# Optimization experiments

Measured on AMD Instinct MI355X. Metric: run time of the kernel, lower is better.

The kernel has to match this reference:

```python
import jax, jax.numpy as jnp
import numpy as np
import math

NUM_WORDS = 8192
WORD_WIDTH = 512
PROJ_WIDTH = 64
NUM_HEADS = 8
SCALE_FACTOR = 100.0

def setup_inputs() -> dict:
    key = jax.random.key(0)
    kx, kq, kk, kv, ko = jax.random.split(key, 5)
    x = jax.random.normal(kx, (NUM_WORDS, WORD_WIDTH), dtype=jnp.float32)
    w_q = jax.random.normal(kq, (WORD_WIDTH, PROJ_WIDTH), dtype=jnp.float32) / SCALE_FACTOR
    w_k = jax.random.normal(kk, (WORD_WIDTH, PROJ_WIDTH), dtype=jnp.float32) / SCALE_FACTOR
    w_v = jax.random.normal(kv, (WORD_WIDTH, PROJ_WIDTH), dtype=jnp.float32) / SCALE_FACTOR
    w_o = jax.random.normal(ko, (WORD_WIDTH, WORD_WIDTH), dtype=jnp.float32)
    return {"x": x, "w_q": w_q, "w_k": w_k, "w_v": w_v, "w_o": w_o}

def reference(x, w_q, w_k, w_v, w_o):
    # Single self-attention head (all 8 heads in the source share the same weights).
    q = x @ w_q            # [N, P]
    k = x @ w_k            # [N, P]
    v = x @ w_v            # [N, P]
    scores = jax.nn.softmax((q @ k.T) / jnp.sqrt(jnp.float32(q.shape[1])), axis=1)  # [N, N]
    head = scores @ v      # [N, P]
    # concat of NUM_HEADS identical head outputs along dim=1
    concat = jnp.tile(head, (1, NUM_HEADS))  # [N, NUM_HEADS*P]
    return concat @ w_o    # [N, WORD_WIDTH]
```

## Files before the change

kernel.cpp:

```cpp
#include <hip/hip_runtime.h>
#include <stdint.h>

#define N_WORDS 8192
#define LOG2E_8 0.18033688011112043f

typedef __attribute__((ext_vector_type(8))) short short8;
typedef __attribute__((ext_vector_type(4))) float f32x4;
typedef __attribute__((ext_vector_type(2))) __fp16 pkhalf2;
typedef __attribute__((ext_vector_type(4))) _Float16 half4;
typedef __attribute__((ext_vector_type(8))) _Float16 half8;

__device__ __forceinline__ unsigned short f32_to_bf16(float f) {
    union { float f; unsigned u; } v; v.f = f;
    unsigned u = v.u;
    return (unsigned short)((u + 0x7FFFu + ((u >> 16) & 1u)) >> 16);
}

__device__ __forceinline__ unsigned short f32_to_f16(float f) {
    union { _Float16 h; unsigned short u; } cv;
    cv.h = (_Float16)f;
    return cv.u;
}

__device__ __forceinline__ void async16(const void* g, void* l) {
    __builtin_amdgcn_global_load_lds(
        (const __attribute__((address_space(1))) unsigned int*)g,
        (__attribute__((address_space(3))) unsigned int*)l, 16, 0, 0);
}

__global__ __launch_bounds__(256) void qkv_gemm(
    const float* __restrict__ x,
    const float* __restrict__ wq, const float* __restrict__ wk,
    const float* __restrict__ wv, const float* __restrict__ wo,
    unsigned short* __restrict__ qB, unsigned short* __restrict__ kB,
    unsigned short* __restrict__ vH, float* __restrict__ we)
{
    int t = threadIdx.x;
    int mat = blockIdx.y;

    if (mat == 3) {
        int i = blockIdx.x * 256 + t;
        int p = i >> 9;
        int j = i & 511;
        float s = 0.0f;
#pragma unroll
        for (int h = 0; h < 8; ++h) s += wo[(size_t)(h * 64 + p) * 512 + j];
        we[i] = s;
        return;
    }

    __shared__ __align__(16) unsigned short ldsX[64 * 72];
    __shared__ __align__(16) unsigned short ldsW[64 * 72];

    int mt = blockIdx.x;
    const float* w = (mat == 0) ? wq : (mat == 1) ? wk : wv;

    int wvid = t >> 6, lane = t & 63;
    int lq = lane & 15, quad = lane >> 4;

    f32x4 acc[4];
#pragma unroll
    for (int nt = 0; nt < 4; ++nt) acc[nt] = (f32x4){0.f, 0.f, 0.f, 0.f};

    float4 xr[4];
    float wr[16];
    int wn = t & 63, wkbs = (t >> 6) * 16;

    {
        int k0 = 0;
#pragma unroll
        for (int j2 = 0; j2 < 4; ++j2) {
            int i = t + j2 * 256;
            int row = i >> 4, c4 = (i & 15) * 4;
            xr[j2] = *(const float4*)(x + (size_t)(mt * 64 + row) * 512 + k0 + c4);
        }
#pragma unroll
        for (int kk = 0; kk < 16; ++kk)
            wr[kk] = w[(size_t)(k0 + wkbs + kk) * 64 + wn];
    }

    for (int kb = 0; kb < 8; ++kb) {
        __syncthreads();
#pragma unroll
        for (int j2 = 0; j2 < 4; ++j2) {
            int i = t + j2 * 256;
            int row = i >> 4, c4 = (i & 15) * 4;
            unsigned p0 = f32_to_bf16(xr[j2].x) | ((unsigned)f32_to_bf16(xr[j2].y) << 16);
            unsigned p1 = f32_to_bf16(xr[j2].z) | ((unsigned)f32_to_bf16(xr[j2].w) << 16);
            *(uint2*)(&ldsX[row * 72 + c4]) = make_uint2(p0, p1);
        }
#pragma unroll
        for (int kk = 0; kk < 16; kk += 2) {
            unsigned p = f32_to_bf16(wr[kk]) | ((unsigned)f32_to_bf16(wr[kk + 1]) << 16);
            *(unsigned*)(&ldsW[wn * 72 + wkbs + kk]) = p;
        }
        __syncthreads();

        if (kb < 7) {
            int k0 = (kb + 1) * 64;
#pragma unroll
            for (int j2 = 0; j2 < 4; ++j2) {
                int i = t + j2 * 256;
                int row = i >> 4, c4 = (i & 15) * 4;
                xr[j2] = *(const float4*)(x + (size_t)(mt * 64 + row) * 512 + k0 + c4);
            }
#pragma unroll
            for (int kk = 0; kk < 16; ++kk)
                wr[kk] = w[(size_t)(k0 + wkbs + kk) * 64 + wn];
        }

        int m = wvid * 16 + lq;
        short8 a0 = *(const short8*)(&ldsX[m * 72 + quad * 8]);
        short8 a1 = *(const short8*)(&ldsX[m * 72 + 32 + quad * 8]);
#pragma unroll
        for (int nt = 0; nt < 4; ++nt) {
            short8 b0 = *(const short8*)(&ldsW[(nt * 16 + lq) * 72 + quad * 8]);
            short8 b1 = *(const short8*)(&ldsW[(nt * 16 + lq) * 72 + 32 + quad * 8]);
            acc[nt] = __builtin_amdgcn_mfma_f32_16x16x32_bf16(a0, b0, acc[nt], 0, 0, 0);
            acc[nt] = __builtin_amdgcn_mfma_f32_16x16x32_bf16(a1, b1, acc[nt], 0, 0, 0);
        }
    }

    int mrow_base = mt * 64 + wvid * 16;
#pragma unroll
    for (int nt = 0; nt < 4; ++nt) {
#pragma unroll
        for (int r = 0; r < 4; ++r) {
            int row = mrow_base + quad * 4 + r;
            int n = nt * 16 + lq;
            float v = acc[nt][r];
            if (mat == 0) {
                v *= LOG2E_8;
                int col = ((((n >> 3) ^ (row & 7)) << 3)) | (n & 7);
                qB[(size_t)row * 64 + col] = f32_to_bf16(v);
            } else if (mat == 1) {
                int col = ((((n >> 3) ^ (row & 7)) << 3)) | (n & 7);
                kB[(size_t)row * 64 + col] = f32_to_bf16(v);
            } else {
                int rs = (row & ~63) | (((((row >> 3) & 7) ^ (n & 7)) << 3)) | (row & 7);
                vH[(size_t)n * N_WORDS + rs] = f32_to_f16(v);
            }
        }
    }
}

__global__ __launch_bounds__(256) void attn_kernel(
    const unsigned short* __restrict__ qB,
    const unsigned short* __restrict__ kB,
    const unsigned short* __restrict__ vH,
    float* __restrict__ pO, float* __restrict__ pl, int nk)
{
    __shared__ __align__(16) unsigned short ldsK[2][128 * 64];
    __shared__ __align__(16) unsigned short ldsV[2][64 * 128];

    int t = threadIdx.x;
    int wvid = t >> 6, lane = t & 63;
    int lq = lane & 15, quad = lane >> 4;
    int mbase = blockIdx.x * 128 + wvid * 32;
    int n0 = blockIdx.y * nk;

    short8 qf[2][2];
#pragma unroll
    for (int qs = 0; qs < 2; ++qs) {
        int row = mbase + qs * 16 + lq;
        const unsigned short* qr = qB + (size_t)row * 64;
        int s7 = row & 7;
        qf[qs][0] = *(const short8*)(qr + ((quad ^ s7) << 3));
        qf[qs][1] = *(const short8*)(qr + (((4 + quad) ^ s7) << 3));
    }

    f32x4 oacc[2][4];
#pragma unroll
    for (int qs = 0; qs < 2; ++qs)
#pragma unroll
        for (int vt = 0; vt < 4; ++vt) oacc[qs][vt] = (f32x4){0.f, 0.f, 0.f, 0.f};
    f32x4 lacc[2];
    lacc[0] = (f32x4){0.f, 0.f, 0.f, 0.f};
    lacc[1] = (f32x4){0.f, 0.f, 0.f, 0.f};

    const half8 ones = {(_Float16)1.f, (_Float16)1.f, (_Float16)1.f, (_Float16)1.f,
                        (_Float16)1.f, (_Float16)1.f, (_Float16)1.f, (_Float16)1.f};

    auto stage = [&](int buf, int nb) {
        const char* gK = (const char*)kB + (size_t)nb * 128;
#pragma unroll
        for (int i = 0; i < 4; ++i) {
            int L0 = (wvid * 4 + i) * 64;
            async16(gK + (size_t)(L0 + lane) * 16, (char*)ldsK[buf] + (size_t)L0 * 16);
        }
#pragma unroll
        for (int i = 0; i < 4; ++i) {
            int L0 = (wvid * 4 + i) * 64;
            int L = L0 + lane;
            int vcol = L >> 4, ct = L & 15;
            const char* src = (const char*)vH + (size_t)vcol * 16384 +
                              (size_t)nb * 2 + ((ct >> 3) << 7) + ((ct & 7) << 4);
            async16(src, (char*)ldsV[buf] + (size_t)L0 * 16);
        }
    };

    int tiles = nk >> 7;
    stage(0, n0);
    int cur = 0;

    for (int tt = 0; tt < tiles; ++tt) {
        __syncthreads();
        if (tt + 1 < tiles) stage(cur ^ 1, n0 + (tt + 1) * 128);

        __builtin_amdgcn_s_setprio(1);
        const unsigned short* K = ldsK[cur];
        const unsigned short* V = ldsV[cur];

#pragma unroll
        for (int u = 0; u < 4; ++u) {
            f32x4 st[2][2];
#pragma unroll
            for (int h = 0; h < 2; ++h) {
                int nt = 2 * u + h;
                int s7 = lq & 7;
                const unsigned short* kr = K + (nt * 16 + lq) * 64;
                short8 a0 = *(const short8*)(kr + ((quad ^ s7) << 3));
                short8 a1 = *(const short8*)(kr + (((4 + quad) ^ s7) << 3));
                f32x4 s0 = (f32x4){0.f, 0.f, 0.f, 0.f};
                f32x4 s1 = (f32x4){0.f, 0.f, 0.f, 0.f};
                s0 = __builtin_amdgcn_mfma_f32_16x16x32_bf16(a0, qf[0][0], s0, 0, 0, 0);
                s0 = __builtin_amdgcn_mfma_f32_16x16x32_bf16(a1, qf[0][1], s0, 0, 0, 0);
                s1 = __builtin_amdgcn_mfma_f32_16x16x32_bf16(a0, qf[1][0], s1, 0, 0, 0);
                s1 = __builtin_amdgcn_mfma_f32_16x16x32_bf16(a1, qf[1][1], s1, 0, 0, 0);
                st[h][0] = s0;
                st[h][1] = s1;
            }

            union { half8 v8; pkhalf2 v2[4]; } pa[2];
#pragma unroll
            for (int qs = 0; qs < 2; ++qs) {
#pragma unroll
                for (int h = 0; h < 2; ++h) {
                    float e0 = exp2f(st[h][qs][0]);
                    float e1 = exp2f(st[h][qs][1]);
                    float e2 = exp2f(st[h][qs][2]);
                    float e3 = exp2f(st[h][qs][3]);
                    pa[qs].v2[h * 2 + 0] = __builtin_amdgcn_cvt_pkrtz(e0, e1);
                    pa[qs].v2[h * 2 + 1] = __builtin_amdgcn_cvt_pkrtz(e2, e3);
                }
                lacc[qs] = __builtin_amdgcn_mfma_f32_16x16x32_f16(
                    pa[qs].v8, ones, lacc[qs], 0, 0, 0);
            }

            int ct0 = 4 * u + (quad >> 1);
            int off = (quad & 1) * 4;
#pragma unroll
            for (int vt = 0; vt < 4; ++vt) {
                int vcol = vt * 16 + lq;
                int cs0 = (ct0 & 8) | ((ct0 & 7) ^ (vcol & 7));
                int ct1 = ct0 + 2;
                int cs1 = (ct1 & 8) | ((ct1 & 7) ^ (vcol & 7));
                union { half8 v8; half4 v4[2]; } vb;
                vb.v4[0] = *(const half4*)(V + vcol * 128 + (cs0 << 3) + off);
                vb.v4[1] = *(const half4*)(V + vcol * 128 + (cs1 << 3) + off);
                oacc[0][vt] = __builtin_amdgcn_mfma_f32_16x16x32_f16(
                    pa[0].v8, vb.v8, oacc[0][vt], 0, 0, 0);
                oacc[1][vt] = __builtin_amdgcn_mfma_f32_16x16x32_f16(
                    pa[1].v8, vb.v8, oacc[1][vt], 0, 0, 0);
            }
        }
        __builtin_amdgcn_s_setprio(0);
        cur ^= 1;
    }

    size_t obase = (size_t)blockIdx.y * N_WORDS;
    if (lq == 0) {
#pragma unroll
        for (int qs = 0; qs < 2; ++qs)
#pragma unroll
            for (int r = 0; r < 4; ++r)
                pl[obase + mbase + qs * 16 + quad * 4 + r] = lacc[qs][r];
    }
#pragma unroll
    for (int qs = 0; qs < 2; ++qs)
#pragma unroll
        for (int vt = 0; vt < 4; ++vt)
#pragma unroll
            for (int r = 0; r < 4; ++r) {
                int row = mbase + qs * 16 + quad * 4 + r;
                pO[(obase + row) * 64 + vt * 16 + lq] = oacc[qs][vt][r];
            }
}

__global__ __launch_bounds__(256) void out_kernel(
    const float* __restrict__ pO, const float* __restrict__ pl,
    const float* __restrict__ we, float* __restrict__ out, int S)
{
    __shared__ __align__(16) float ldsHT[64 * 16];
    int t = threadIdx.x;
    int r0 = blockIdx.x * 16;

#pragma unroll
    for (int j = 0; j < 4; ++j) {
        int i = t + j * 256;
        int row = i >> 6, d = i & 63;
        float so = 0.f, sl = 0.f;
        for (int s = 0; s < S; ++s) {
            so += pO[((size_t)s * N_WORDS + r0 + row) * 64 + d];
            sl += pl[(size_t)s * N_WORDS + r0 + row];
        }
        ldsHT[d * 16 + row] = so / sl;
    }
    __syncthreads();

    int w = t >> 6, l = t & 63;
    int cg = w & 1, rg = w >> 1;
    int j0 = cg * 256 + l * 4;

    float4 acc[8];
#pragma unroll
    for (int rr = 0; rr < 8; ++rr) acc[rr] = (float4){0.f, 0.f, 0.f, 0.f};

    for (int k = 0; k < 64; ++k) {
        float4 wv = *(const float4*)(we + (size_t)k * 512 + j0);
        float4 h0 = *(const float4*)(ldsHT + k * 16 + rg * 8);
        float4 h1 = *(const float4*)(ldsHT + k * 16 + rg * 8 + 4);
        float hr[8] = {h0.x, h0.y, h0.z, h0.w, h1.x, h1.y, h1.z, h1.w};
#pragma unroll
        for (int rr = 0; rr < 8; ++rr) {
            acc[rr].x = fmaf(hr[rr], wv.x, acc[rr].x);
            acc[rr].y = fmaf(hr[rr], wv.y, acc[rr].y);
            acc[rr].z = fmaf(hr[rr], wv.z, acc[rr].z);
            acc[rr].w = fmaf(hr[rr], wv.w, acc[rr].w);
        }
    }

#pragma unroll
    for (int rr = 0; rr < 8; ++rr) {
        int row = r0 + rg * 8 + rr;
        *(float4*)(out + (size_t)row * 512 + j0) = acc[rr];
    }
}

extern "C" void kernel_launch(void* const* d_in, const int* in_sizes, int n_in,
                              void* d_out, int out_size, void* d_ws, size_t ws_size,
                              hipStream_t stream)
{
    const float* x  = (const float*)d_in[0];
    const float* wq = (const float*)d_in[1];
    const float* wk = (const float*)d_in[2];
    const float* wv = (const float*)d_in[3];
    const float* wo = (const float*)d_in[4];
    float* out = (float*)d_out;

    char* ws = (char*)d_ws;
    unsigned short* qB = (unsigned short*)(ws);
    unsigned short* kB = (unsigned short*)(ws + 1048576);
    unsigned short* vH = (unsigned short*)(ws + 2097152);
    float* we   = (float*)(ws + 3145728);
    float* pl   = (float*)(ws + 5373952);
    float* pO   = (float*)(ws + 5636096);

    int S = (ws_size >= (size_t)(5636096) + 8u * 2097152u) ? 8 : 4;
    int nk = N_WORDS / S;

    hipLaunchKernelGGL(qkv_gemm, dim3(128, 4), dim3(256), 0, stream,
                       x, wq, wk, wv, wo, qB, kB, vH, we);
    hipLaunchKernelGGL(attn_kernel, dim3(64, S), dim3(256), 0, stream,
                       qB, kB, vH, pO, pl, nk);
    hipLaunchKernelGGL(out_kernel, dim3(512), dim3(256), 0, stream,
                       pO, pl, we, out, S);
}
```

Baseline: 131.8 us.

## Use fp16 partials and MFMA output projection, scalar row-sum in attention

Attention partial outputs and the folded output weight are now stored as fp16 instead of fp32, halving workspace traffic between kernels. The output projection is rewritten from scalar FMA loops to f16 MFMA using a transposed weight layout. In the attention loop, the softmax row sum becomes scalar adds plus a final cross-lane shuffle reduction, replacing the extra MFMA against a ones vector. This lowers precision of the intermediates and output matmul, and adds VALU adds in the inner loop.

New measurement: 130.3 us. No clear change (-1.2%).

```diff
diff --git a/kernel.cpp b/kernel.cpp
--- a/kernel.cpp
+++ b/kernel.cpp
@@ -33,7 +33,7 @@
     const float* __restrict__ wq, const float* __restrict__ wk,
     const float* __restrict__ wv, const float* __restrict__ wo,
     unsigned short* __restrict__ qB, unsigned short* __restrict__ kB,
-    unsigned short* __restrict__ vH, float* __restrict__ we)
+    unsigned short* __restrict__ vH, unsigned short* __restrict__ weT)
 {
     int t = threadIdx.x;
     int mat = blockIdx.y;
@@ -45,7 +45,7 @@
         float s = 0.0f;
 #pragma unroll
         for (int h = 0; h < 8; ++h) s += wo[(size_t)(h * 64 + p) * 512 + j];
-        we[i] = s;
+        weT[(size_t)j * 64 + p] = f32_to_f16(s);
         return;
     }
 
@@ -148,7 +148,7 @@
     const unsigned short* __restrict__ qB,
     const unsigned short* __restrict__ kB,
     const unsigned short* __restrict__ vH,
-    float* __restrict__ pO, float* __restrict__ pl, int nk)
+    unsigned short* __restrict__ pOh, float* __restrict__ pl, int nk)
 {
     __shared__ __align__(16) unsigned short ldsK[2][128 * 64];
     __shared__ __align__(16) unsigned short ldsV[2][64 * 128];
@@ -174,12 +174,7 @@
     for (int qs = 0; qs < 2; ++qs)
 #pragma unroll
         for (int vt = 0; vt < 4; ++vt) oacc[qs][vt] = (f32x4){0.f, 0.f, 0.f, 0.f};
-    f32x4 lacc[2];
-    lacc[0] = (f32x4){0.f, 0.f, 0.f, 0.f};
-    lacc[1] = (f32x4){0.f, 0.f, 0.f, 0.f};
-
-    const half8 ones = {(_Float16)1.f, (_Float16)1.f, (_Float16)1.f, (_Float16)1.f,
-                        (_Float16)1.f, (_Float16)1.f, (_Float16)1.f, (_Float16)1.f};
+    float lsum0 = 0.f, lsum1 = 0.f;
 
     auto stage = [&](int buf, int nb) {
         const char* gK = (const char*)kB + (size_t)nb * 128;
@@ -233,18 +228,21 @@
 
             union { half8 v8; pkhalf2 v2[4]; } pa[2];
 #pragma unroll
-            for (int qs = 0; qs < 2; ++qs) {
-#pragma unroll
-                for (int h = 0; h < 2; ++h) {
-                    float e0 = exp2f(st[h][qs][0]);
-                    float e1 = exp2f(st[h][qs][1]);
-                    float e2 = exp2f(st[h][qs][2]);
-                    float e3 = exp2f(st[h][qs][3]);
-                    pa[qs].v2[h * 2 + 0] = __builtin_amdgcn_cvt_pkrtz(e0, e1);
-                    pa[qs].v2[h * 2 + 1] = __builtin_amdgcn_cvt_pkrtz(e2, e3);
-                }
-                lacc[qs] = __builtin_amdgcn_mfma_f32_16x16x32_f16(
-                    pa[qs].v8, ones, lacc[qs], 0, 0, 0);
+            for (int h = 0; h < 2; ++h) {
+                float e0 = exp2f(st[h][0][0]);
+                float e1 = exp2f(st[h][0][1]);
+                float e2 = exp2f(st[h][0][2]);
+                float e3 = exp2f(st[h][0][3]);
+                lsum0 += (e0 + e1) + (e2 + e3);
+                pa[0].v2[h * 2 + 0] = __builtin_amdgcn_cvt_pkrtz(e0, e1);
+                pa[0].v2[h * 2 + 1] = __builtin_amdgcn_cvt_pkrtz(e2, e3);
+                float f0 = exp2f(st[h][1][0]);
+                float f1 = exp2f(st[h][1][1]);
+                float f2 = exp2f(st[h][1][2]);
+                float f3 = exp2f(st[h][1][3]);
+                lsum1 += (f0 + f1) + (f2 + f3);
+                pa[1].v2[h * 2 + 0] = __builtin_amdgcn_cvt_pkrtz(f0, f1);
+                pa[1].v2[h * 2 + 1] = __builtin_amdgcn_cvt_pkrtz(f2, f3);
             }
 
             int ct0 = 4 * u + (quad >> 1);
@@ -268,13 +266,13 @@
         cur ^= 1;
     }
 
+    lsum0 += __shfl_xor(lsum0, 16); lsum0 += __shfl_xor(lsum0, 32);
+    lsum1 += __shfl_xor(lsum1, 16); lsum1 += __shfl_xor(lsum1, 32);
+
     size_t obase = (size_t)blockIdx.y * N_WORDS;
-    if (lq == 0) {
-#pragma unroll
-        for (int qs = 0; qs < 2; ++qs)
-#pragma unroll
-            for (int r = 0; r < 4; ++r)
-                pl[obase + mbase + qs * 16 + quad * 4 + r] = lacc[qs][r];
+    if (quad == 0) {
+        pl[obase + mbase + lq] = lsum0;
+        pl[obase + mbase + 16 + lq] = lsum1;
     }
 #pragma unroll
     for (int qs = 0; qs < 2; ++qs)
@@ -283,17 +281,18 @@
 #pragma unroll
             for (int r = 0; r < 4; ++r) {
                 int row = mbase + qs * 16 + quad * 4 + r;
-                pO[(obase + row) * 64 + vt * 16 + lq] = oacc[qs][vt][r];
+                pOh[(obase + row) * 64 + vt * 16 + lq] = f32_to_f16(oacc[qs][vt][r]);
             }
 }
 
 __global__ __launch_bounds__(256) void out_kernel(
-    const float* __restrict__ pO, const float* __restrict__ pl,
-    const float* __restrict__ we, float* __restrict__ out, int S)
+    const unsigned short* __restrict__ pOh, const float* __restrict__ pl,
+    const unsigned short* __restrict__ weT, float* __restrict__ out, int S)
 {
-    __shared__ __align__(16) float ldsHT[64 * 16];
+    __shared__ __align__(16) _Float16 ldsH[16 * 72];
     int t = threadIdx.x;
     int r0 = blockIdx.x * 16;
+    const _Float16* pOf = (const _Float16*)pOh;
 
 #pragma unroll
     for (int j = 0; j < 4; ++j) {
@@ -301,39 +300,32 @@
         int row = i >> 6, d = i & 63;
         float so = 0.f, sl = 0.f;
         for (int s = 0; s < S; ++s) {
-            so += pO[((size_t)s * N_WORDS + r0 + row) * 64 + d];
+            so += (float)pOf[((size_t)s * N_WORDS + r0 + row) * 64 + d];
             sl += pl[(size_t)s * N_WORDS + r0 + row];
         }
-        ldsHT[d * 16 + row] = so / sl;
+        ldsH[row * 72 + d] = (_Float16)(so / sl);
     }
     __syncthreads();
 
-    int w = t >> 6, l = t & 63;
-    int cg = w & 1, rg = w >> 1;
-    int j0 = cg * 256 + l * 4;
-
-    float4 acc[8];
-#pragma unroll
-    for (int rr = 0; rr < 8; ++rr) acc[rr] = (float4){0.f, 0.f, 0.f, 0.f};
-
-    for (int k = 0; k < 64; ++k) {
-        float4 wv = *(const float4*)(we + (size_t)k * 512 + j0);
-        float4 h0 = *(const float4*)(ldsHT + k * 16 + rg * 8);
-        float4 h1 = *(const float4*)(ldsHT + k * 16 + rg * 8 + 4);
-        float hr[8] = {h0.x, h0.y, h0.z, h0.w, h1.x, h1.y, h1.z, h1.w};
-#pragma unroll
-        for (int rr = 0; rr < 8; ++rr) {
-            acc[rr].x = fmaf(hr[rr], wv.x, acc[rr].x);
-            acc[rr].y = fmaf(hr[rr], wv.y, acc[rr].y);
-            acc[rr].z = fmaf(hr[rr], wv.z, acc[rr].z);
-            acc[rr].w = fmaf(hr[rr], wv.w, acc[rr].w);
-        }
-    }
-
-#pragma unroll
-    for (int rr = 0; rr < 8; ++rr) {
-        int row = r0 + rg * 8 + rr;
-        *(float4*)(out + (size_t)row * 512 + j0) = acc[rr];
+    int wv = t >> 6, lane = t & 63;
+    int lq = lane & 15, quad = lane >> 4;
+
+    half8 a0 = *(const half8*)(&ldsH[lq * 72 + quad * 8]);
+    half8 a1 = *(const half8*)(&ldsH[lq * 72 + 32 + quad * 8]);
+    const _Float16* wT = (const _Float16*)weT;
+
+#pragma unroll
+    for (int ntl = 0; ntl < 8; ++ntl) {
+        int nt = wv * 8 + ntl;
+        const _Float16* wrow = wT + (size_t)(nt * 16 + lq) * 64;
+        half8 b0 = *(const half8*)(wrow + quad * 8);
+        half8 b1 = *(const half8*)(wrow + 32 + quad * 8);
+        f32x4 acc = (f32x4){0.f, 0.f, 0.f, 0.f};
+        acc = __builtin_amdgcn_mfma_f32_16x16x32_f16(a0, b0, acc, 0, 0, 0);
+        acc = __builtin_amdgcn_mfma_f32_16x16x32_f16(a1, b1, acc, 0, 0, 0);
+#pragma unroll
+        for (int r = 0; r < 4; ++r)
+            out[(size_t)(r0 + quad * 4 + r) * 512 + nt * 16 + lq] = acc[r];
     }
 }
 
@@ -349,20 +341,20 @@
     float* out = (float*)d_out;
 
     char* ws = (char*)d_ws;
-    unsigned short* qB = (unsigned short*)(ws);
-    unsigned short* kB = (unsigned short*)(ws + 1048576);
-    unsigned short* vH = (unsigned short*)(ws + 2097152);
-    float* we   = (float*)(ws + 3145728);
-    float* pl   = (float*)(ws + 5373952);
-    float* pO   = (float*)(ws + 5636096);
-
-    int S = (ws_size >= (size_t)(5636096) + 8u * 2097152u) ? 8 : 4;
+    unsigned short* qB  = (unsigned short*)(ws);
+    unsigned short* kB  = (unsigned short*)(ws + 1048576);
+    unsigned short* vH  = (unsigned short*)(ws + 2097152);
+    unsigned short* weT = (unsigned short*)(ws + 3145728);
+    float* pl           = (float*)(ws + 3211264);
+    unsigned short* pOh = (unsigned short*)(ws + 3473408);
+
+    int S = (ws_size >= (size_t)3473408 + 8u * 1048576u) ? 8 : 4;
     int nk = N_WORDS / S;
 
     hipLaunchKernelGGL(qkv_gemm, dim3(128, 4), dim3(256), 0, stream,
-                       x, wq, wk, wv, wo, qB, kB, vH, we);
+                       x, wq, wk, wv, wo, qB, kB, vH, weT);
     hipLaunchKernelGGL(attn_kernel, dim3(64, S), dim3(256), 0, stream,
-                       qB, kB, vH, pO, pl, nk);
+                       qB, kB, vH, pOh, pl, nk);
     hipLaunchKernelGGL(out_kernel, dim3(512), dim3(256), 0, stream,
-                       pO, pl, we, out, S);
-}
+                       pOh, pl, weT, out, S);
+}
```
